# Kernel tuning notes

Hardware: AMD Instinct MI355X
Metric: run time of the kernel (lower is better)

The kernel has to match this reference:

```python
import jax, jax.numpy as jnp
import numpy as np

B, S, P, D, H = 2, 1024, 1024, 2048, 16
DH = D // H
QMAX = 127.0


def quantize(x):
    # per-tensor abs-max int8 quantization, matching torch quantize(bits=8)
    scale = jnp.max(jnp.abs(x)) / QMAX
    x_q = jnp.clip(jnp.round(x / scale), -128.0, 127.0).astype(jnp.int8)
    return x_q, scale


def dequantize(x_q, scale):
    return x_q.astype(jnp.float32) * scale


def setup_inputs() -> dict:
    key = jax.random.key(0)
    ks = jax.random.split(key, 12)
    sd = 1.0 / np.sqrt(D)
    inp = {
        'hidden_states': jax.random.normal(ks[0], (B, S, D), jnp.float32),
        'Wq': jax.random.normal(ks[1], (D, D), jnp.float32) * sd,
        'bq': jnp.zeros((D,), jnp.float32),
        'Wk': jax.random.normal(ks[2], (D, D), jnp.float32) * sd,
        'bk': jnp.zeros((D,), jnp.float32),
        'Wv': jax.random.normal(ks[3], (D, D), jnp.float32) * sd,
        'bv': jnp.zeros((D,), jnp.float32),
        'Wo': jax.random.normal(ks[4], (D, D), jnp.float32) * sd,
        'bo': jnp.zeros((D,), jnp.float32),
        'past_k_q': jax.random.randint(ks[5], (B, P, D), -128, 128).astype(jnp.int8),
        'past_k_scale': jnp.float32(0.03),
        'past_v_q': jax.random.randint(ks[6], (B, P, D), -128, 128).astype(jnp.int8),
        'past_v_scale': jnp.float32(0.02),
    }
    return inp


def attention(h, k, v, Wq, bq, Wo, bo):
    # standard causal MHA; query positions are offset by the cache length P
    T = k.shape[1]  # P + S
    q = (h @ Wq + bq).reshape(B, S, H, DH)
    kh = k.reshape(B, T, H, DH)
    vh = v.reshape(B, T, H, DH)
    scores = jnp.einsum('bshd,bthd->bhst', q, kh) / np.sqrt(DH)  # [B,H,S,T]
    causal = jnp.arange(T)[None, :] <= (P + jnp.arange(S))[:, None]  # [S,T]
    scores = jnp.where(causal[None, None], scores, jnp.float32(-1e30))
    attn = jax.nn.softmax(scores, axis=-1)
    out = jnp.einsum('bhst,bthd->bshd', attn, vh).reshape(B, S, D)
    return out @ Wo + bo


def reference(hidden_states, Wq, bq, Wk, bk, Wv, bv, Wo, bo,
              past_k_q, past_k_scale, past_v_q, past_v_scale):
    k = hidden_states @ Wk + bk  # [B,S,D]
    v = hidden_states @ Wv + bv
    k_q, k_scale = quantize(k)
    v_q, v_scale = quantize(v)
    # dequantize cached KV and concat along the sequence dim (dim=1)
    k_prev = dequantize(past_k_q, past_k_scale)
    v_prev = dequantize(past_v_q, past_v_scale)
    k_full = jnp.concatenate([k_prev, k], axis=1)  # [B,P+S,D]
    v_full = jnp.concatenate([v_prev, v], axis=1)
    out = attention(hidden_states, k_full, v_full, Wq, bq, Wo, bo)
    return out, k_q, k_scale, v_q, v_scale
```

## Files before the change

kernel.cpp:

```cpp
#include <hip/hip_runtime.h>

#define SOFT_SCALE 0.08838834764831845f
#define BSD 4194304
#define NELEM 4194304

typedef __attribute__((ext_vector_type(4))) float    f32x4;
typedef __attribute__((ext_vector_type(8))) short    bf16x8;
typedef __attribute__((ext_vector_type(4))) short    bf16x4;
typedef __attribute__((ext_vector_type(4))) unsigned u32x4;

__device__ __forceinline__ float bs2f(short s) {
    unsigned u = ((unsigned)(unsigned short)s) << 16;
    return __builtin_bit_cast(float, u);
}
__device__ __forceinline__ short f2bs(float f) {
    unsigned u = __builtin_bit_cast(unsigned, f);
    unsigned r = (u + 0x7fffu + ((u >> 16) & 1u)) >> 16;
    return (short)r;
}

__device__ __forceinline__ void stage16(const short* g, short* l) {
#if __has_builtin(__builtin_amdgcn_global_load_lds)
    __builtin_amdgcn_global_load_lds(
        (const __attribute__((address_space(1))) void*)g,
        (__attribute__((address_space(3))) void*)l, 16, 0, 0);
#else
    *(bf16x8*)l = *(const bf16x8*)g;
#endif
}

__global__ void probe_init(const int* __restrict__ q, float* __restrict__ scal) {
    const int lane = threadIdx.x;
    int bad = 0;
#pragma unroll
    for (int i = 0; i < 4; ++i) {
        const int v = q[i * 64 + lane];
        bad |= (v < -128 || v > 127) ? 1 : 0;
    }
    const int anybad = __any(bad);
    if (lane == 0) ((int*)scal)[2] = anybad ? 0 : 1;
    if (lane == 1) scal[0] = 0.f;
    if (lane == 2) scal[1] = 0.f;
}

__global__ void conv_bf16(const float* __restrict__ X, short* __restrict__ Y) {
    const int stride = gridDim.x * blockDim.x;
    for (int i = blockIdx.x * blockDim.x + threadIdx.x; i < NELEM / 8; i += stride) {
        const int e = i * 8;
        f32x4 a = *(const f32x4*)&X[e];
        f32x4 b = *(const f32x4*)&X[e + 4];
        bf16x8 o;
        o[0] = f2bs(a[0]); o[1] = f2bs(a[1]); o[2] = f2bs(a[2]); o[3] = f2bs(a[3]);
        o[4] = f2bs(b[0]); o[5] = f2bs(b[1]); o[6] = f2bs(b[2]); o[7] = f2bs(b[3]);
        *(bf16x8*)&Y[e] = o;
    }
}

__global__ __launch_bounds__(256) void transpose_conv(const float* __restrict__ W0,
                                                      const float* __restrict__ W1,
                                                      const float* __restrict__ W2,
                                                      short* __restrict__ WT) {
    __shared__ __align__(16) short Tl[64 * 68];
    const float* W = blockIdx.z == 0 ? W0 : (blockIdx.z == 1 ? W1 : W2);
    short* out = WT + (long)blockIdx.z * 4194304;
    const int tid = threadIdx.x;
    const int n0 = blockIdx.x * 64, k0 = blockIdx.y * 64;
#pragma unroll
    for (int i = 0; i < 4; ++i) {
        const int e = i * 1024 + tid * 4;
        const int r = e >> 6, c = e & 63;
        f32x4 f = *(const f32x4*)&W[(long)(k0 + r) * 2048 + n0 + c];
        bf16x4 s4 = { f2bs(f[0]), f2bs(f[1]), f2bs(f[2]), f2bs(f[3]) };
        *(bf16x4*)&Tl[r * 68 + c] = s4;
    }
    __syncthreads();
#pragma unroll
    for (int i = 0; i < 4; ++i) {
        const int e = i * 1024 + tid * 4;
        const int nr = e >> 6, kk = e & 63;
        bf16x4 o = { Tl[(kk + 0) * 68 + nr], Tl[(kk + 1) * 68 + nr],
                     Tl[(kk + 2) * 68 + nr], Tl[(kk + 3) * 68 + nr] };
        *(bf16x4*)&out[(long)(n0 + nr) * 2048 + k0 + kk] = o;
    }
}

__global__ void dequant_kernel(const void* __restrict__ pk, const void* __restrict__ pv,
                               const float* __restrict__ psk, const float* __restrict__ psv,
                               short* __restrict__ Kf, short* __restrict__ Vf,
                               const int* __restrict__ wsflag) {
    const int z = blockIdx.z;
    const void* src = z ? pv : pk;
    const float sc = z ? *psv : *psk;
    short* dst = z ? Vf : Kf;
    const int flag = wsflag[2];
    const int stride = gridDim.x * blockDim.x;
    for (int i = blockIdx.x * blockDim.x + threadIdx.x; i < NELEM / 8; i += stride) {
        const int e = i * 8;
        int vals[8];
        if (flag) {
            const int* s = (const int*)src + e;
            *(int4*)&vals[0] = *(const int4*)&s[0];
            *(int4*)&vals[4] = *(const int4*)&s[4];
        } else {
            const int2 wv = *(const int2*)((const char*)src + e);
#pragma unroll
            for (int j = 0; j < 4; ++j) vals[j] = (int)(signed char)(wv.x >> (8 * j));
#pragma unroll
            for (int j = 0; j < 4; ++j) vals[4 + j] = (int)(signed char)(wv.y >> (8 * j));
        }
        bf16x8 o;
#pragma unroll
        for (int j = 0; j < 8; ++j) o[j] = f2bs((float)vals[j] * sc);
        *(bf16x8*)&dst[e + ((e >> 21) << 21)] = o;
    }
}

__global__ __launch_bounds__(256, 3) void gemm_m97(
    const short* __restrict__ A,
    const short* __restrict__ Bt0, const short* __restrict__ Bt1, const short* __restrict__ Bt2,
    const float* __restrict__ bi0, const float* __restrict__ bi1, const float* __restrict__ bi2,
    void* __restrict__ o0, void* __restrict__ o1, void* __restrict__ o2,
    float* __restrict__ scal, int mode_sgl, float scale_sgl, int amax_sgl) {
    __shared__ __align__(16) short Al[2][4096];
    __shared__ __align__(16) short Bl[2][4096];
    const int nbx = gridDim.x, nby = gridDim.y, nbz = gridDim.z;
    const int nwg = nbx * nby * nbz;
    const int orig = blockIdx.x + nbx * (blockIdx.y + nby * blockIdx.z);
    const int cpx = nwg >> 3;
    int swz = (orig & 7) * cpx + (orig >> 3);
    const int bx = swz % nbx; swz /= nbx;
    const int by = swz % nby;
    const int bz = swz / nby;

    const short* Bt   = bz == 0 ? Bt0 : (bz == 1 ? Bt1 : Bt2);
    const float* bias = bz == 0 ? bi0 : (bz == 1 ? bi1 : bi2);
    void* outp        = bz == 0 ? o0  : (bz == 1 ? o1  : o2);
    int mode, amx; float scl;
    if (nbz == 3) { mode = (bz == 0) ? 1 : 2; scl = (bz == 0) ? SOFT_SCALE : 1.f;
                    amx = (bz == 0) ? -1 : (bz - 1); }
    else          { mode = mode_sgl; scl = scale_sgl; amx = amax_sgl; }

    const int tid = threadIdx.x, lane = tid & 63, w = tid >> 6;
    const int wm = w >> 1, wn = w & 1, l4 = lane >> 4, ln = lane & 15;
    const int m0 = by * 128, n0 = bx * 128;

    const int srow = tid >> 2;
    const int cswz = ((tid & 3) ^ ((srow >> 1) & 3)) * 8;
    const short* gA0 = A  + (long)(m0 + srow) * 2048 + cswz;
    const short* gA1 = gA0 + 64 * 2048;
    const short* gB0 = Bt + (long)(n0 + srow) * 2048 + cswz;
    const short* gB1 = gB0 + 64 * 2048;

    f32x4 acc[4][4];
#pragma unroll
    for (int mi = 0; mi < 4; ++mi)
#pragma unroll
        for (int ni = 0; ni < 4; ++ni) acc[mi][ni] = (f32x4){0, 0, 0, 0};

#define STAGE_G(buf, ko)                                   \
    do {                                                   \
        stage16(gA0 + (ko), &Al[buf][tid * 8]);            \
        stage16(gA1 + (ko), &Al[buf][2048 + tid * 8]);     \
        stage16(gB0 + (ko), &Bl[buf][tid * 8]);            \
        stage16(gB1 + (ko), &Bl[buf][2048 + tid * 8]);     \
    } while (0)

    STAGE_G(0, 0);
    STAGE_G(1, 32);

    const int gsw = (ln >> 1) & 3;
    for (int kt = 0; kt < 64; ++kt) {
        if (kt < 63) asm volatile("s_waitcnt vmcnt(4)" ::: "memory");
        else         asm volatile("s_waitcnt vmcnt(0)" ::: "memory");
        __builtin_amdgcn_s_barrier();
        const int cur = kt & 1;
        bf16x8 af[4], bfr[4];
#pragma unroll
        for (int mi = 0; mi < 4; ++mi)
            af[mi] = *(const bf16x8*)&Al[cur][(wm * 64 + mi * 16 + ln) * 32 + (l4 ^ gsw) * 8];
#pragma unroll
        for (int ni = 0; ni < 4; ++ni)
            bfr[ni] = *(const bf16x8*)&Bl[cur][(wn * 64 + ni * 16 + ln) * 32 + (l4 ^ gsw) * 8];
        asm volatile("s_waitcnt lgkmcnt(0)" ::: "memory");
        __builtin_amdgcn_s_barrier();
        if (kt < 62) STAGE_G(cur, (kt + 2) * 32);
        __builtin_amdgcn_s_setprio(1);
#pragma unroll
        for (int mi = 0; mi < 4; ++mi)
#pragma unroll
            for (int ni = 0; ni < 4; ++ni)
                acc[mi][ni] = __builtin_amdgcn_mfma_f32_16x16x32_bf16(
                    af[mi], bfr[ni], acc[mi][ni], 0, 0, 0);
        __builtin_amdgcn_s_setprio(0);
    }
#undef STAGE_G

    float amax = 0.f;
#pragma unroll
    for (int ni = 0; ni < 4; ++ni) {
        const int gn = n0 + wn * 64 + ni * 16 + ln;
        const float bv = bias[gn];
#pragma unroll
        for (int mi = 0; mi < 4; ++mi) {
#pragma unroll
            for (int r = 0; r < 4; ++r) {
                const int gm = m0 + wm * 64 + mi * 16 + l4 * 4 + r;
                const float v = (acc[mi][ni][r] + bv) * scl;
                amax = fmaxf(amax, fabsf(v));
                if (mode == 0) {
                    ((float*)outp)[(long)gm * 2048 + gn] = v;
                } else if (mode == 1) {
                    ((short*)outp)[(long)gm * 2048 + gn] = f2bs(v);
                } else {
                    const int gr = gm + 1024 + ((gm >> 10) << 10);
                    ((short*)outp)[(long)gr * 2048 + gn] = f2bs(v);
                }
            }
        }
    }
    if (amx >= 0) {
#pragma unroll
        for (int o = 32; o > 0; o >>= 1) amax = fmaxf(amax, __shfl_xor(amax, o));
        if (lane == 0)
            atomicMax((unsigned int*)&scal[amx], __builtin_bit_cast(unsigned int, amax));
    }
}

__global__ void quantize_kernel(const short* __restrict__ Kf, const short* __restrict__ Vf,
                                const float* __restrict__ scal, float* __restrict__ out) {
    const int z = blockIdx.z;
    const short* src = z ? Vf : Kf;
    const float mx = scal[z];
    const float scale = mx * (1.f / 127.f);
    const float inv = (mx > 0.f) ? 127.f / mx : 0.f;
    const long ob = z ? (2L * BSD + 1) : (1L * BSD);
    if (blockIdx.x == 0 && threadIdx.x == 0)
        out[z ? (3L * BSD + 1) : (2L * BSD)] = scale;
    const int stride = gridDim.x * blockDim.x;
    for (int i = blockIdx.x * blockDim.x + threadIdx.x; i < NELEM / 4; i += stride) {
        const int e = i * 4;
        const int flat = e + 2097152 + ((e >> 21) << 21);
        bf16x4 x4 = *(const bf16x4*)&src[flat];
        float4 q;
        q.x = fminf(127.f, fmaxf(-128.f, rintf(bs2f(x4[0]) * inv)));
        q.y = fminf(127.f, fmaxf(-128.f, rintf(bs2f(x4[1]) * inv)));
        q.z = fminf(127.f, fmaxf(-128.f, rintf(bs2f(x4[2]) * inv)));
        q.w = fminf(127.f, fmaxf(-128.f, rintf(bs2f(x4[3]) * inv)));
        *(float4*)&out[ob + e] = q;
    }
}

__global__ __launch_bounds__(256, 2) void attn_kernel(const short* __restrict__ Q,
                                                      const short* __restrict__ Kf,
                                                      const short* __restrict__ Vf,
                                                      short* __restrict__ O) {
    __shared__ __align__(16) short Kl[64 * 136];
    __shared__ __align__(16) short Vt[128 * 72];
    const int L = blockIdx.x + 16 * (blockIdx.y + 16 * blockIdx.z);
    const int x = L & 7, rr = L >> 3;
    const int qt0 = rr & 15, pgrp = rr >> 4;
    const int p = x + 8 * pgrp;
    const int h = p >> 1, b = p & 1;
    const int qt = (pgrp >= 2) ? (15 - qt0) : qt0;

    const int tid = threadIdx.x, w = tid >> 6, lane = tid & 63;
    const int l4 = lane >> 4, n = lane & 15;
    const int rg = tid >> 4, cg = tid & 15, stc = cg * 8;
    const int sIdx = qt * 64 + w * 16 + n;
    const int qlim = 1024 + sIdx;

    bf16x8 qf[4];
#pragma unroll
    for (int c = 0; c < 4; ++c)
        qf[c] = *(const bf16x8*)&Q[(long)(b * 1024 + sIdx) * 2048 + h * 128 + c * 32 + l4 * 8];

    f32x4 acco[8];
#pragma unroll
    for (int i = 0; i < 8; ++i) acco[i] = (f32x4){0, 0, 0, 0};
    float m_run = -1e30f, l_run = 0.f;

    const short* Kb = Kf + (long)(b * 2048) * 2048 + h * 128;
    const short* Vb = Vf + (long)(b * 2048) * 2048 + h * 128;
    const int nt = 17 + qt;

    bf16x8 kreg[4], vreg[4];
#pragma unroll
    for (int i = 0; i < 4; ++i) kreg[i] = *(const bf16x8*)&Kb[(long)(i * 16 + rg) * 2048 + stc];
#pragma unroll
    for (int i = 0; i < 4; ++i) vreg[i] = *(const bf16x8*)&Vb[(long)(rg * 4 + i) * 2048 + stc];

    for (int t = 0; t < nt; ++t) {
        const int t0 = t * 64;
        __syncthreads();
#pragma unroll
        for (int i = 0; i < 4; ++i)
            *(bf16x8*)&Kl[(i * 16 + rg) * 136 + stc] = kreg[i];
#pragma unroll
        for (int j = 0; j < 8; ++j) {
            const int d = stc + j;
            bf16x4 c4 = { vreg[0][j], vreg[1][j], vreg[2][j], vreg[3][j] };
            *(bf16x4*)&Vt[d * 72 + ((rg ^ ((d >> 3) & 7)) << 2)] = c4;
        }
        if (t + 1 < nt) {
            const int t1 = (t + 1) * 64;
#pragma unroll
            for (int i = 0; i < 4; ++i)
                kreg[i] = *(const bf16x8*)&Kb[(long)(t1 + i * 16 + rg) * 2048 + stc];
#pragma unroll
            for (int i = 0; i < 4; ++i)
                vreg[i] = *(const bf16x8*)&Vb[(long)(t1 + rg * 4 + i) * 2048 + stc];
        }
        __syncthreads();

        float p16[16];
        __builtin_amdgcn_s_setprio(1);
#pragma unroll
        for (int kt = 0; kt < 4; ++kt) {
            f32x4 sc4 = (f32x4){0, 0, 0, 0};
#pragma unroll
            for (int c = 0; c < 4; ++c) {
                bf16x8 kfr = *(const bf16x8*)&Kl[(kt * 16 + n) * 136 + c * 32 + l4 * 8];
                sc4 = __builtin_amdgcn_mfma_f32_16x16x32_bf16(kfr, qf[c], sc4, 0, 0, 0);
            }
#pragma unroll
            for (int r = 0; r < 4; ++r) p16[kt * 4 + r] = sc4[r];
        }
        __builtin_amdgcn_s_setprio(0);
        if (t >= 16) {
#pragma unroll
            for (int i = 0; i < 16; ++i) {
                const int kg = t0 + (i >> 2) * 16 + l4 * 4 + (i & 3);
                if (kg > qlim) p16[i] = -1e30f;
            }
        }

        float tmax = p16[0];
#pragma unroll
        for (int i = 1; i < 16; ++i) tmax = fmaxf(tmax, p16[i]);
        tmax = fmaxf(tmax, __shfl_xor(tmax, 16));
        tmax = fmaxf(tmax, __shfl_xor(tmax, 32));
        if (!__all(tmax <= m_run + 8.f)) {
            const float mnew = fmaxf(m_run, tmax);
            const float fac = __expf(m_run - mnew);
            l_run *= fac;
#pragma unroll
            for (int i = 0; i < 8; ++i) acco[i] *= fac;
            m_run = mnew;
        }
        float tsum = 0.f;
#pragma unroll
        for (int i = 0; i < 16; ++i) { p16[i] = __expf(p16[i] - m_run); tsum += p16[i]; }
        tsum += __shfl_xor(tsum, 16);
        tsum += __shfl_xor(tsum, 32);
        l_run += tsum;

        u32x4 pw0, pw1;
#pragma unroll
        for (int wd = 0; wd < 4; ++wd) {
            unsigned r0, r1;
            asm("v_cvt_pk_bf16_f32 %0, %1, %2" : "=v"(r0) : "v"(p16[2 * wd]), "v"(p16[2 * wd + 1]));
            asm("v_cvt_pk_bf16_f32 %0, %1, %2" : "=v"(r1) : "v"(p16[8 + 2 * wd]), "v"(p16[8 + 2 * wd + 1]));
            pw0[wd] = r0; pw1[wd] = r1;
        }
        bf16x8 pb[2] = { __builtin_bit_cast(bf16x8, pw0), __builtin_bit_cast(bf16x8, pw1) };

        __builtin_amdgcn_s_setprio(1);
#pragma unroll
        for (int dc = 0; dc < 8; ++dc) {
            const int d = dc * 16 + n;
            const int swd = ((d >> 3) & 7) << 2;
#pragma unroll
            for (int k32 = 0; k32 < 2; ++k32) {
                bf16x4 g0 = *(const bf16x4*)&Vt[d * 72 + (k32 * 32 + ((4 * l4) ^ swd))];
                bf16x4 g1 = *(const bf16x4*)&Vt[d * 72 + (k32 * 32 + ((16 + 4 * l4) ^ swd))];
                bf16x8 vf = { g0[0], g0[1], g0[2], g0[3], g1[0], g1[1], g1[2], g1[3] };
                acco[dc] = __builtin_amdgcn_mfma_f32_16x16x32_bf16(vf, pb[k32], acco[dc], 0, 0, 0);
            }
        }
        __builtin_amdgcn_s_setprio(0);
    }

    __syncthreads();
    const float inv = 1.f / l_run;
#pragma unroll
    for (int dc = 0; dc < 8; ++dc)
#pragma unroll
        for (int r = 0; r < 4; ++r)
            Kl[(w * 16 + n) * 136 + dc * 16 + l4 * 4 + r] = f2bs(acco[dc][r] * inv);
    __syncthreads();
#pragma unroll
    for (int i = 0; i < 4; ++i) {
        const int row = i * 4 + (lane >> 4);
        const int col = (lane & 15) * 8;
        bf16x8 ov = *(const bf16x8*)&Kl[(w * 16 + row) * 136 + col];
        *(bf16x8*)&O[(long)(b * 1024 + qt * 64 + w * 16 + row) * 2048 + h * 128 + col] = ov;
    }
}

extern "C" void kernel_launch(void* const* d_in, const int* in_sizes, int n_in,
                              void* d_out, int out_size, void* d_ws, size_t ws_size,
                              hipStream_t stream) {
    const float* h   = (const float*)d_in[0];
    const float* Wq  = (const float*)d_in[1];
    const float* bq  = (const float*)d_in[2];
    const float* Wk  = (const float*)d_in[3];
    const float* bk  = (const float*)d_in[4];
    const float* Wv  = (const float*)d_in[5];
    const float* bv  = (const float*)d_in[6];
    const float* Wo  = (const float*)d_in[7];
    const float* bo  = (const float*)d_in[8];
    const void*  pkq = d_in[9];
    const float* pks = (const float*)d_in[10];
    const void*  pvq = d_in[11];
    const float* pvs = (const float*)d_in[12];
    float* out = (float*)d_out;

    char* ws = (char*)d_ws;
    dim3 blk(256);
    const bool big = (ws_size >= 75500000ull);

    if (big) {
        float* scal  = (float*)ws;
        short* hbf   = (short*)(ws + 256);
        short* WT3   = (short*)(ws + 256 + 1L * 8388608);
        short* Qbf   = (short*)(ws + 256 + 4L * 8388608);
        short* Kfull = (short*)(ws + 256 + 5L * 8388608);
        short* Vfull = (short*)(ws + 256 + 5L * 8388608 + 16777216);
        short* attnb = hbf;

        probe_init<<<1, 64, 0, stream>>>((const int*)pkq, scal);
        conv_bf16<<<1024, blk, 0, stream>>>(h, hbf);
        dequant_kernel<<<dim3(256, 1, 2), blk, 0, stream>>>(pkq, pvq, pks, pvs, Kfull, Vfull,
                                                            (const int*)d_ws);
        transpose_conv<<<dim3(32, 32, 3), blk, 0, stream>>>(Wq, Wk, Wv, WT3);
        gemm_m97<<<dim3(16, 16, 3), blk, 0, stream>>>(hbf, WT3, WT3 + 4194304, WT3 + 8388608,
                                                      bq, bk, bv, Qbf, Kfull, Vfull,
                                                      scal, 0, 1.f, -1);
        quantize_kernel<<<dim3(256, 1, 2), blk, 0, stream>>>(Kfull, Vfull, scal, out);
        attn_kernel<<<dim3(16, 16, 2), blk, 0, stream>>>(Qbf, Kfull, Vfull, attnb);
        transpose_conv<<<dim3(32, 32, 1), blk, 0, stream>>>(Wo, Wo, Wo, WT3);
        gemm_m97<<<dim3(16, 16, 1), blk, 0, stream>>>(attnb, WT3, WT3, WT3, bo, bo, bo,
                                                      out, out, out, scal, 0, 1.f, -1);
    } else {
        float* scal  = (float*)ws;
        short* hbf   = (short*)(ws + 256);
        short* WT    = (short*)(ws + 256 + 1L * 8388608);
        short* Qbf   = (short*)(ws + 256 + 2L * 8388608);
        short* Kfull = (short*)(ws + 256 + 3L * 8388608);
        short* Vfull = (short*)(ws + 256 + 3L * 8388608 + 16777216);
        short* attnb = hbf;

        probe_init<<<1, 64, 0, stream>>>((const int*)pkq, scal);
        conv_bf16<<<1024, blk, 0, stream>>>(h, hbf);
        dequant_kernel<<<dim3(256, 1, 2), blk, 0, stream>>>(pkq, pvq, pks, pvs, Kfull, Vfull,
                                                            (const int*)d_ws);
        transpose_conv<<<dim3(32, 32, 1), blk, 0, stream>>>(Wk, Wk, Wk, WT);
        gemm_m97<<<dim3(16, 16, 1), blk, 0, stream>>>(hbf, WT, WT, WT, bk, bk, bk,
                                                      Kfull, Kfull, Kfull, scal, 2, 1.f, 0);
        transpose_conv<<<dim3(32, 32, 1), blk, 0, stream>>>(Wv, Wv, Wv, WT);
        gemm_m97<<<dim3(16, 16, 1), blk, 0, stream>>>(hbf, WT, WT, WT, bv, bv, bv,
                                                      Vfull, Vfull, Vfull, scal, 2, 1.f, 1);
        quantize_kernel<<<dim3(256, 1, 2), blk, 0, stream>>>(Kfull, Vfull, scal, out);
        transpose_conv<<<dim3(32, 32, 1), blk, 0, stream>>>(Wq, Wq, Wq, WT);
        gemm_m97<<<dim3(16, 16, 1), blk, 0, stream>>>(hbf, WT, WT, WT, bq, bq, bq,
                                                      Qbf, Qbf, Qbf, scal, 1, SOFT_SCALE, -1);
        attn_kernel<<<dim3(16, 16, 2), blk, 0, stream>>>(Qbf, Kfull, Vfull, attnb);
        transpose_conv<<<dim3(32, 32, 1), blk, 0, stream>>>(Wo, Wo, Wo, WT);
        gemm_m97<<<dim3(16, 16, 1), blk, 0, stream>>>(attnb, WT, WT, WT, bo, bo, bo,
                                                      out, out, out, scal, 0, 1.f, -1);
    }
}
```

Measured before the change: 229.6 us.

## Simplify GEMM double-buffer pipeline and add narrower-tile output projection kernel

The main GEMM drops its two-stage-ahead prefetch with split barriers and priority hints. It now uses a simpler double buffer that issues the next tile's loads before computing the current one, then waits for all loads and syncs once per iteration. Launch bounds drop from 3 to 2 blocks per CU. A new gemm_wo kernel with 128x64 tiles (512 blocks) replaces the 256-block launch for the Wo projection to fill more CUs. The risk is less latency hiding, since each iteration now waits on all outstanding loads, and lower occupancy in the QKV GEMMs.

```diff
diff --git a/kernel.cpp b/kernel.cpp
--- a/kernel.cpp
+++ b/kernel.cpp
@@ -115,7 +115,7 @@
     }
 }
 
-__global__ __launch_bounds__(256, 3) void gemm_m97(
+__global__ __launch_bounds__(256, 2) void gemm_m97(
     const short* __restrict__ A,
     const short* __restrict__ Bt0, const short* __restrict__ Bt1, const short* __restrict__ Bt2,
     const float* __restrict__ bi0, const float* __restrict__ bi1, const float* __restrict__ bi2,
@@ -166,14 +166,12 @@
     } while (0)
 
     STAGE_G(0, 0);
-    STAGE_G(1, 32);
-
+    asm volatile("s_waitcnt vmcnt(0)" ::: "memory");
+    __syncthreads();
+    int cur = 0;
     const int gsw = (ln >> 1) & 3;
     for (int kt = 0; kt < 64; ++kt) {
-        if (kt < 63) asm volatile("s_waitcnt vmcnt(4)" ::: "memory");
-        else         asm volatile("s_waitcnt vmcnt(0)" ::: "memory");
-        __builtin_amdgcn_s_barrier();
-        const int cur = kt & 1;
+        if (kt < 63) STAGE_G(cur ^ 1, (kt + 1) * 32);
         bf16x8 af[4], bfr[4];
 #pragma unroll
         for (int mi = 0; mi < 4; ++mi)
@@ -181,17 +179,15 @@
 #pragma unroll
         for (int ni = 0; ni < 4; ++ni)
             bfr[ni] = *(const bf16x8*)&Bl[cur][(wn * 64 + ni * 16 + ln) * 32 + (l4 ^ gsw) * 8];
-        asm volatile("s_waitcnt lgkmcnt(0)" ::: "memory");
-        __builtin_amdgcn_s_barrier();
-        if (kt < 62) STAGE_G(cur, (kt + 2) * 32);
-        __builtin_amdgcn_s_setprio(1);
 #pragma unroll
         for (int mi = 0; mi < 4; ++mi)
 #pragma unroll
             for (int ni = 0; ni < 4; ++ni)
                 acc[mi][ni] = __builtin_amdgcn_mfma_f32_16x16x32_bf16(
                     af[mi], bfr[ni], acc[mi][ni], 0, 0, 0);
-        __builtin_amdgcn_s_setprio(0);
+        asm volatile("s_waitcnt vmcnt(0)" ::: "memory");
+        __syncthreads();
+        cur ^= 1;
     }
 #undef STAGE_G
 
@@ -223,6 +219,79 @@
         for (int o = 32; o > 0; o >>= 1) amax = fmaxf(amax, __shfl_xor(amax, o));
         if (lane == 0)
             atomicMax((unsigned int*)&scal[amx], __builtin_bit_cast(unsigned int, amax));
+    }
+}
+
+__global__ __launch_bounds__(256, 2) void gemm_wo(const short* __restrict__ A,
+                                                  const short* __restrict__ Bt,
+                                                  const float* __restrict__ bias,
+                                                  float* __restrict__ outp) {
+    __shared__ __align__(16) short Al[2][4096];
+    __shared__ __align__(16) short Bl[2][2048];
+    const int orig = blockIdx.x + 32 * blockIdx.y;
+    const int swz = (orig & 7) * 64 + (orig >> 3);
+    const int bx = swz & 31, by = swz >> 5;
+    const int tid = threadIdx.x, lane = tid & 63, w = tid >> 6;
+    const int wm = w >> 1, wn = w & 1, l4 = lane >> 4, ln = lane & 15;
+    const int m0 = by * 128, n0 = bx * 64;
+
+    const int srow = tid >> 2;
+    const int cswz = ((tid & 3) ^ ((srow >> 1) & 3)) * 8;
+    const short* gA0 = A  + (long)(m0 + srow) * 2048 + cswz;
+    const short* gA1 = gA0 + 64 * 2048;
+    const short* gB0 = Bt + (long)(n0 + srow) * 2048 + cswz;
+
+    f32x4 acc[4][2];
+#pragma unroll
+    for (int mi = 0; mi < 4; ++mi)
+#pragma unroll
+        for (int ni = 0; ni < 2; ++ni) acc[mi][ni] = (f32x4){0, 0, 0, 0};
+
+#define STAGE_W(buf, ko)                                   \
+    do {                                                   \
+        stage16(gA0 + (ko), &Al[buf][tid * 8]);            \
+        stage16(gA1 + (ko), &Al[buf][2048 + tid * 8]);     \
+        stage16(gB0 + (ko), &Bl[buf][tid * 8]);            \
+    } while (0)
+
+    STAGE_W(0, 0);
+    asm volatile("s_waitcnt vmcnt(0)" ::: "memory");
+    __syncthreads();
+    int cur = 0;
+    const int gsw = (ln >> 1) & 3;
+    for (int kt = 0; kt < 64; ++kt) {
+        if (kt < 63) STAGE_W(cur ^ 1, (kt + 1) * 32);
+        bf16x8 af[4], bfr[2];
+#pragma unroll
+        for (int mi = 0; mi < 4; ++mi)
+            af[mi] = *(const bf16x8*)&Al[cur][(wm * 64 + mi * 16 + ln) * 32 + (l4 ^ gsw) * 8];
+#pragma unroll
+        for (int ni = 0; ni < 2; ++ni)
+            bfr[ni] = *(const bf16x8*)&Bl[cur][(wn * 32 + ni * 16 + ln) * 32 + (l4 ^ gsw) * 8];
+#pragma unroll
+        for (int mi = 0; mi < 4; ++mi)
+#pragma unroll
+            for (int ni = 0; ni < 2; ++ni)
+                acc[mi][ni] = __builtin_amdgcn_mfma_f32_16x16x32_bf16(
+                    af[mi], bfr[ni], acc[mi][ni], 0, 0, 0);
+        asm volatile("s_waitcnt vmcnt(0)" ::: "memory");
+        __syncthreads();
+        cur ^= 1;
+    }
+#undef STAGE_W
+
+#pragma unroll
+    for (int ni = 0; ni < 2; ++ni) {
+        const int gn = n0 + wn * 32 + ni * 16 + ln;
+        const float bv = bias[gn];
+#pragma unroll
+        for (int mi = 0; mi < 4; ++mi) {
+#pragma unroll
+            for (int r = 0; r < 4; ++r) {
+                const int gm = m0 + wm * 64 + mi * 16 + l4 * 4 + r;
+                outp[(long)gm * 2048 + gn] = acc[mi][ni][r] + bv;
+            }
+        }
     }
 }
 
@@ -439,8 +508,7 @@
         quantize_kernel<<<dim3(256, 1, 2), blk, 0, stream>>>(Kfull, Vfull, scal, out);
         attn_kernel<<<dim3(16, 16, 2), blk, 0, stream>>>(Qbf, Kfull, Vfull, attnb);
         transpose_conv<<<dim3(32, 32, 1), blk, 0, stream>>>(Wo, Wo, Wo, WT3);
-        gemm_m97<<<dim3(16, 16, 1), blk, 0, stream>>>(attnb, WT3, WT3, WT3, bo, bo, bo,
-                                                      out, out, out, scal, 0, 1.f, -1);
+        gemm_wo<<<dim3(32, 16), blk, 0, stream>>>(attnb, WT3, bo, out);
     } else {
         float* scal  = (float*)ws;
         short* hbf   = (short*)(ws + 256);
@@ -466,7 +534,6 @@
                                                       Qbf, Qbf, Qbf, scal, 1, SOFT_SCALE, -1);
         attn_kernel<<<dim3(16, 16, 2), blk, 0, stream>>>(Qbf, Kfull, Vfull, attnb);
         transpose_conv<<<dim3(32, 32, 1), blk, 0, stream>>>(Wo, Wo, Wo, WT);
-        gemm_m97<<<dim3(16, 16, 1), blk, 0, stream>>>(attnb, WT, WT, WT, bo, bo, bo,
-                                                      out, out, out, scal, 0, 1.f, -1);
-    }
-}
+        gemm_wo<<<dim3(32, 16), blk, 0, stream>>>(attnb, WT, bo, out);
+    }
+}
```

After: 230.6 us. Within noise of the previous version (+0.4%).
